# Performance work log

Hardware: AMD Instinct MI355X
Metric: run time of the kernel (lower is better)

Reference implementation:

```python
import jax, jax.numpy as jnp
import numpy as np

N_NODES = 50000
N_EDGES = 500000
D_IN = 128
HID = 128
OUT = 2
N_REL = 4
BN_EPS = 1e-5


def setup_inputs() -> dict:
    key = jax.random.key(0)
    ks = jax.random.split(key, 14)
    s_in = 1.0 / np.sqrt(D_IN)
    s_h = 1.0 / np.sqrt(HID)
    return {
        "x": jax.random.normal(ks[0], (N_NODES, D_IN), jnp.float32),
        "edge_index": jax.random.randint(ks[1], (N_REL, 2, N_EDGES), 0, N_NODES, jnp.int32),
        "W1": jax.random.normal(ks[2], (N_REL, D_IN, HID), jnp.float32) * s_in,
        "b1": jax.random.normal(ks[3], (N_REL, HID), jnp.float32) * s_in,
        "W2": jax.random.normal(ks[4], (N_REL, HID, HID), jnp.float32) * s_h,
        "b2": jax.random.normal(ks[5], (N_REL, HID), jnp.float32) * s_h,
        "bn_gamma": jnp.ones((HID,), jnp.float32),
        "bn_beta": jnp.zeros((HID,), jnp.float32),
        "lin1_W": jax.random.normal(ks[6], (HID, HID), jnp.float32) * s_h,
        "lin1_b": jax.random.normal(ks[7], (HID,), jnp.float32) * s_h,
        "lin2_W": jax.random.normal(ks[8], (HID, OUT), jnp.float32) * s_h,
        "lin2_b": jax.random.normal(ks[9], (OUT,), jnp.float32) * s_h,
    }


def _gcn(x, ei, W, b):
    # GCNConv: D^-1/2 (A + I) D^-1/2 (X W) + b
    n = x.shape[0]
    h = x @ W                                    # [N, H]
    loops = jnp.arange(n, dtype=ei.dtype)
    src = jnp.concatenate([ei[0], loops])        # add self loops
    dst = jnp.concatenate([ei[1], loops])
    deg = jax.ops.segment_sum(jnp.ones(dst.shape, h.dtype), dst, num_segments=n)
    dinv = jnp.where(deg > 0, jax.lax.rsqrt(deg), 0.0)
    norm = dinv[src] * dinv[dst]                 # [E+N]
    msg = h[src] * norm[:, None]                 # gather + scale
    return jax.ops.segment_sum(msg, dst, num_segments=n) + b


def _hetero(x, edge_index, W, b):
    # HeteroConv with aggr='sum' over the 4 relation types (same src/dst node type)
    out = _gcn(x, edge_index[0], W[0], b[0])
    for r in range(1, N_REL):
        out = out + _gcn(x, edge_index[r], W[r], b[r])
    return out


def reference(x, edge_index, W1, b1, W2, b2, bn_gamma, bn_beta, lin1_W, lin1_b, lin2_W, lin2_b):
    h = jax.nn.relu(_hetero(x, edge_index, W1, b1))
    h = jax.nn.relu(_hetero(h, edge_index, W2, b2))
    # BatchNorm1d (batch statistics, biased variance)
    mean = h.mean(axis=0)
    var = h.var(axis=0)
    h = (h - mean) * jax.lax.rsqrt(var + BN_EPS) * bn_gamma + bn_beta
    h = jax.nn.relu(h @ lin1_W + lin1_b)
    # dropout is identity in eval
    return h @ lin2_W + lin2_b
```

## Files before the change

kernel.cpp:

```cpp
#include <hip/hip_runtime.h>
#include <math.h>

#define NN 50000
#define NE 500000
#define NREL 4
#define D 128
#define RSZ 512
#define NRANGE 98
#define NBK (NREL * NRANGE)
#define BCAP 6144
#define NCH 128
#define CH 3907
#define FCAP 96
#define CAST_BLKS 6250
static constexpr float BN_EPS = 1e-5f;

typedef __attribute__((ext_vector_type(8))) short short8;
typedef __attribute__((ext_vector_type(4))) float f32x4;

__device__ __forceinline__ float bf2f(unsigned short u) {
    return __uint_as_float(((unsigned)u) << 16);
}
__device__ __forceinline__ unsigned short f2bf(float f) {
    unsigned x = __float_as_uint(f);
    return (unsigned short)((x + 0x7FFFu + ((x >> 16) & 1u)) >> 16);
}

__global__ __launch_bounds__(256) void k_pre(const float* __restrict__ x,
                                             const float* __restrict__ W1, const float* __restrict__ W2,
                                             const float* __restrict__ l1W, const float* __restrict__ b1,
                                             const float* __restrict__ b2,
                                             unsigned short* __restrict__ xb,
                                             unsigned short* __restrict__ Wt1,
                                             unsigned short* __restrict__ Wt2,
                                             unsigned short* __restrict__ Wt3,
                                             float* __restrict__ bs1, float* __restrict__ bs2,
                                             float* __restrict__ bnsum) {
    int blk = blockIdx.x, tid = threadIdx.x;
    if (blk < CAST_BLKS) {
        int i = blk * 256 + tid;
        float4 v = *(const float4*)(x + (size_t)i * 4);
        unsigned short u[4] = {f2bf(v.x), f2bf(v.y), f2bf(v.z), f2bf(v.w)};
        *(ushort4*)(xb + (size_t)i * 4) = *(ushort4*)u;
    } else if (blk < CAST_BLKS + 256) {
        int i = (blk - CAST_BLKS) * 256 + tid;
        int kk = i & 511, n = i >> 9;
        Wt1[n * 512 + kk] = f2bf(W1[kk * 128 + n]);
        Wt2[n * 512 + kk] = f2bf(W2[kk * 128 + n]);
    } else if (blk < CAST_BLKS + 320) {
        int i = (blk - CAST_BLKS - 256) * 256 + tid;
        int kk = i & 127, n = i >> 7;
        Wt3[n * 128 + kk] = f2bf(l1W[kk * 128 + n]);
    } else {
        if (tid < 128) {
            bs1[tid] = b1[tid] + b1[128 + tid] + b1[256 + tid] + b1[384 + tid];
            bs2[tid] = b2[tid] + b2[128 + tid] + b2[256 + tid] + b2[384 + tid];
        }
        bnsum[tid] = 0.f;
    }
}

__global__ __launch_bounds__(256) void k_bin(const int* __restrict__ ei,
                                             int* __restrict__ frag,
                                             int* __restrict__ cntg) {
    int c = blockIdx.x, r = blockIdx.y;
    const int* srcp = ei + r * 2 * NE;
    const int* dstp = srcp + NE;
    __shared__ int bins[NRANGE * FCAP];
    __shared__ int cnt[NRANGE];
    int tid = threadIdx.x;
    for (int i = tid; i < NRANGE; i += 256) cnt[i] = 0;
    __syncthreads();
    int e0 = c * CH, e1 = min(e0 + CH, NE);
    for (int e = e0 + tid; e < e1; e += 256) {
        int d = dstp[e];
        int s = srcp[e];
        int q = d >> 9;
        int pos = atomicAdd(&cnt[q], 1);
        if (pos < FCAP) bins[q * FCAP + pos] = s | ((d & 511) << 16);
    }
    __syncthreads();
    int w = tid >> 6, lane = tid & 63;
    for (int q = w; q < NRANGE; q += 4) {
        int k = min(cnt[q], FCAP);
        int gbase = ((r * NRANGE + q) * NCH + c) * FCAP;
        for (int i = lane; i < k; i += 64) frag[gbase + i] = bins[q * FCAP + i];
    }
    for (int q = tid; q < NRANGE; q += 256) cntg[(r * NRANGE + q) * NCH + c] = min(cnt[q], FCAP);
}

__global__ __launch_bounds__(512) void k_sortb(const int* __restrict__ frag,
                                               const int* __restrict__ cntg,
                                               unsigned short* __restrict__ csr,
                                               int* __restrict__ rstart,
                                               int* __restrict__ rend,
                                               float* __restrict__ dinv) {
    int q = blockIdx.x, r = blockIdx.y;
    int blk = r * NRANGE + q;
    int n0 = q * RSZ;
    int nrows = min(RSZ, NN - n0);
    __shared__ int cnts[NCH], cbase[NCH];
    __shared__ int stage[BCAP];
    __shared__ unsigned short csr_s[BCAP];
    __shared__ int hist[RSZ], off[RSZ], cnt2[RSZ];
    int tid = threadIdx.x;
    hist[tid] = 0;
    cnt2[tid] = 0;
    if (tid < NCH) cnts[tid] = cntg[blk * NCH + tid];
    __syncthreads();
    if (tid < NCH) cbase[tid] = cnts[tid];
    __syncthreads();
    for (int d = 1; d < NCH; d <<= 1) {
        int t = 0;
        if (tid < NCH && tid >= d) t = cbase[tid - d];
        __syncthreads();
        if (tid < NCH) cbase[tid] += t;
        __syncthreads();
    }
    if (tid < NCH) cbase[tid] -= cnts[tid];
    __syncthreads();
    int tot = cbase[NCH - 1] + cnts[NCH - 1];
    {
        int g = tid >> 2, l = tid & 3;
        int k = cnts[g], cb = cbase[g];
        int gbase = (blk * NCH + g) * FCAP;
        for (int i = l; i < k; i += 4)
            if (cb + i < BCAP) stage[cb + i] = frag[gbase + i];
    }
    __syncthreads();
    if (tot > BCAP) tot = BCAP;
    for (int i = tid; i < tot; i += 512) atomicAdd(&hist[(stage[i] >> 16) & 511], 1);
    __syncthreads();
    int h = hist[tid];
    if (tid < nrows) dinv[r * NN + n0 + tid] = rsqrtf((float)(h + 1));
    off[tid] = h;
    __syncthreads();
    for (int d = 1; d < RSZ; d <<= 1) {
        int t = (tid >= d) ? off[tid - d] : 0;
        __syncthreads();
        off[tid] += t;
        __syncthreads();
    }
    int excl = off[tid] - h;
    __syncthreads();
    off[tid] = excl;
    int base = blk * BCAP;
    if (tid < nrows) {
        rstart[r * NN + n0 + tid] = base + excl;
        rend[r * NN + n0 + tid] = base + excl + h;
    }
    __syncthreads();
    for (int i = tid; i < tot; i += 512) {
        int v = stage[i];
        int dl = (v >> 16) & 511;
        int p = atomicAdd(&cnt2[dl], 1);
        csr_s[off[dl] + p] = (unsigned short)(v & 0xFFFF);
    }
    __syncthreads();
    for (int i = tid; i < tot; i += 512) csr[base + i] = csr_s[i];
}

__global__ __launch_bounds__(256) void k_agg(const unsigned short* __restrict__ in,
                                             const unsigned short* __restrict__ csr,
                                             const int* __restrict__ rstart,
                                             const int* __restrict__ rend,
                                             const float* __restrict__ dinv,
                                             unsigned short* __restrict__ Acat) {
    int r = blockIdx.y;
    int wave = threadIdx.x >> 6, lane = threadIdx.x & 63;
    int n = blockIdx.x * 4 + wave;
    if (n >= NN) return;
    const float* dv = dinv + r * NN;
    int start = rstart[r * NN + n], end = rend[r * NN + n];
    int half = lane >> 5;
    int c = lane & 31;
    const ushort4* in4 = (const ushort4*)in;
    float a0 = 0.f, a1 = 0.f, a2 = 0.f, a3 = 0.f;
    int e = start + half;
    for (; e + 2 < end; e += 4) {
        int s0 = csr[e], s1 = csr[e + 2];
        float w0 = dv[s0], w1 = dv[s1];
        ushort4 u0 = in4[s0 * 32 + c];
        ushort4 u1 = in4[s1 * 32 + c];
        a0 = fmaf(bf2f(u0.x), w0, a0); a1 = fmaf(bf2f(u0.y), w0, a1);
        a2 = fmaf(bf2f(u0.z), w0, a2); a3 = fmaf(bf2f(u0.w), w0, a3);
        a0 = fmaf(bf2f(u1.x), w1, a0); a1 = fmaf(bf2f(u1.y), w1, a1);
        a2 = fmaf(bf2f(u1.z), w1, a2); a3 = fmaf(bf2f(u1.w), w1, a3);
    }
    if (e < end) {
        int s = csr[e];
        float w = dv[s];
        ushort4 u = in4[s * 32 + c];
        a0 = fmaf(bf2f(u.x), w, a0); a1 = fmaf(bf2f(u.y), w, a1);
        a2 = fmaf(bf2f(u.z), w, a2); a3 = fmaf(bf2f(u.w), w, a3);
    }
    a0 += __shfl_xor(a0, 32); a1 += __shfl_xor(a1, 32);
    a2 += __shfl_xor(a2, 32); a3 += __shfl_xor(a3, 32);
    float wn = dv[n];
    ushort4 us = in4[n * 32 + c];
    unsigned short ob[4];
    ob[0] = f2bf(wn * fmaf(bf2f(us.x), wn, a0));
    ob[1] = f2bf(wn * fmaf(bf2f(us.y), wn, a1));
    ob[2] = f2bf(wn * fmaf(bf2f(us.z), wn, a2));
    ob[3] = f2bf(wn * fmaf(bf2f(us.w), wn, a3));
    if (half == 0)
        *(ushort4*)(Acat + (size_t)n * 512 + r * 128 + 4 * c) = *(ushort4*)ob;
}

template <int K, bool STATS>
__global__ __launch_bounds__(256) void k_mm(const unsigned short* __restrict__ A,
                                            const unsigned short* __restrict__ Bt,
                                            const float* __restrict__ bias,
                                            unsigned short* __restrict__ C,
                                            float* __restrict__ bnsum) {
    int tid = threadIdx.x;
    int w = tid >> 6, lane = tid & 63;
    int ln = lane & 15, quad = lane >> 4;
    int mwave = blockIdx.x * 256 + w * 64;

    f32x4 acc[4][8];
#pragma unroll
    for (int a = 0; a < 4; a++)
#pragma unroll
        for (int b = 0; b < 8; b++) acc[a][b] = (f32x4){0.f, 0.f, 0.f, 0.f};

    size_t arow[4];
#pragma unroll
    for (int mf = 0; mf < 4; mf++) {
        int m = mwave + mf * 16 + ln;
        arow[mf] = (size_t)min(m, NN - 1) * K;
    }
    size_t brow[8];
#pragma unroll
    for (int nf = 0; nf < 8; nf++) brow[nf] = (size_t)(nf * 16 + ln) * K;

    for (int k0 = 0; k0 < K; k0 += 32) {
        int kof = k0 + quad * 8;
        short8 af[4], bf[8];
#pragma unroll
        for (int mf = 0; mf < 4; mf++) af[mf] = *(const short8*)(A + arow[mf] + kof);
#pragma unroll
        for (int nf = 0; nf < 8; nf++) bf[nf] = *(const short8*)(Bt + brow[nf] + kof);
#pragma unroll
        for (int mf = 0; mf < 4; mf++)
#pragma unroll
            for (int nf = 0; nf < 8; nf++)
                acc[mf][nf] = __builtin_amdgcn_mfma_f32_16x16x32_bf16(af[mf], bf[nf], acc[mf][nf], 0, 0, 0);
    }

    float bs[8];
#pragma unroll
    for (int nf = 0; nf < 8; nf++) bs[nf] = bias[nf * 16 + ln];
    float sn[8], qn[8];
#pragma unroll
    for (int nf = 0; nf < 8; nf++) { sn[nf] = 0.f; qn[nf] = 0.f; }

#pragma unroll
    for (int mf = 0; mf < 4; mf++)
#pragma unroll
        for (int nf = 0; nf < 8; nf++)
#pragma unroll
            for (int rg = 0; rg < 4; rg++) {
                int m = mwave + mf * 16 + quad * 4 + rg;
                if (m < NN) {
                    float v = fmaxf(acc[mf][nf][rg] + bs[nf], 0.f);
                    if (STATS) { sn[nf] += v; qn[nf] += v * v; }
                    C[(size_t)m * 128 + nf * 16 + ln] = f2bf(v);
                }
            }

    if (STATS) {
#pragma unroll
        for (int nf = 0; nf < 8; nf++) {
            float s = sn[nf], q = qn[nf];
            s += __shfl_xor(s, 16); s += __shfl_xor(s, 32);
            q += __shfl_xor(q, 16); q += __shfl_xor(q, 32);
            if (quad == 0) {
                unsafeAtomicAdd(&bnsum[nf * 16 + ln], s);
                unsafeAtomicAdd(&bnsum[128 + nf * 16 + ln], q);
            }
        }
    }
}

__global__ __launch_bounds__(256) void k_final(const unsigned short* __restrict__ R2,
                                               const float* __restrict__ bnsum,
                                               const float* __restrict__ gamma,
                                               const float* __restrict__ beta,
                                               const unsigned short* __restrict__ Wt3,
                                               const float* __restrict__ l1b,
                                               const float* __restrict__ l2W,
                                               const float* __restrict__ l2b,
                                               float* __restrict__ out) {
    __shared__ float bnp_s[256];
    int tid = threadIdx.x;
    if (tid < 128) {
        float mean = bnsum[tid] / (float)NN;
        float var = bnsum[128 + tid] / (float)NN - mean * mean;
        float sc = gamma[tid] * rsqrtf(var + BN_EPS);
        bnp_s[tid] = sc;
        bnp_s[128 + tid] = beta[tid] - mean * sc;
    }
    __syncthreads();
    int w = tid >> 6, lane = tid & 63;
    int ln = lane & 15, quad = lane >> 4;
    int mwave = blockIdx.x * 256 + w * 64;

    f32x4 acc[4][8];
#pragma unroll
    for (int a = 0; a < 4; a++)
#pragma unroll
        for (int b = 0; b < 8; b++) acc[a][b] = (f32x4){0.f, 0.f, 0.f, 0.f};

    size_t arow[4];
#pragma unroll
    for (int mf = 0; mf < 4; mf++) {
        int m = mwave + mf * 16 + ln;
        arow[mf] = (size_t)min(m, NN - 1) * 128;
    }
    size_t brow[8];
#pragma unroll
    for (int nf = 0; nf < 8; nf++) brow[nf] = (size_t)(nf * 16 + ln) * 128;

    for (int k0 = 0; k0 < 128; k0 += 32) {
        int kof = k0 + quad * 8;
        float scv[8], shv[8];
#pragma unroll
        for (int j = 0; j < 8; j++) {
            scv[j] = bnp_s[kof + j];
            shv[j] = bnp_s[128 + kof + j];
        }
        short8 af[4], bf[8];
#pragma unroll
        for (int mf = 0; mf < 4; mf++) {
            short8 rv = *(const short8*)(R2 + arow[mf] + kof);
            unsigned short ab[8];
#pragma unroll
            for (int j = 0; j < 8; j++)
                ab[j] = f2bf(bf2f((unsigned short)rv[j]) * scv[j] + shv[j]);
            af[mf] = *(short8*)ab;
        }
#pragma unroll
        for (int nf = 0; nf < 8; nf++) bf[nf] = *(const short8*)(Wt3 + brow[nf] + kof);
#pragma unroll
        for (int mf = 0; mf < 4; mf++)
#pragma unroll
            for (int nf = 0; nf < 8; nf++)
                acc[mf][nf] = __builtin_amdgcn_mfma_f32_16x16x32_bf16(af[mf], bf[nf], acc[mf][nf], 0, 0, 0);
    }

    float b1v[8], w0[8], w1[8];
#pragma unroll
    for (int nf = 0; nf < 8; nf++) {
        int n = nf * 16 + ln;
        b1v[nf] = l1b[n];
        w0[nf] = l2W[n * 2];
        w1[nf] = l2W[n * 2 + 1];
    }
    float ob0 = l2b[0], ob1 = l2b[1];
#pragma unroll
    for (int mf = 0; mf < 4; mf++)
#pragma unroll
        for (int rg = 0; rg < 4; rg++) {
            float p0 = 0.f, p1 = 0.f;
#pragma unroll
            for (int nf = 0; nf < 8; nf++) {
                float y = fmaxf(acc[mf][nf][rg] + b1v[nf], 0.f);
                p0 += y * w0[nf];
                p1 += y * w1[nf];
            }
            p0 += __shfl_xor(p0, 1); p0 += __shfl_xor(p0, 2);
            p0 += __shfl_xor(p0, 4); p0 += __shfl_xor(p0, 8);
            p1 += __shfl_xor(p1, 1); p1 += __shfl_xor(p1, 2);
            p1 += __shfl_xor(p1, 4); p1 += __shfl_xor(p1, 8);
            int m = mwave + mf * 16 + quad * 4 + rg;
            if (ln == 0 && m < NN) {
                out[(size_t)m * 2 + 0] = p0 + ob0;
                out[(size_t)m * 2 + 1] = p1 + ob1;
            }
        }
}

extern "C" void kernel_launch(void* const* d_in, const int* in_sizes, int n_in,
                              void* d_out, int out_size, void* d_ws, size_t ws_size,
                              hipStream_t stream) {
    const float* x = (const float*)d_in[0];
    const int* ei = (const int*)d_in[1];
    const float* W1 = (const float*)d_in[2];
    const float* b1 = (const float*)d_in[3];
    const float* W2 = (const float*)d_in[4];
    const float* b2 = (const float*)d_in[5];
    const float* gamma = (const float*)d_in[6];
    const float* beta = (const float*)d_in[7];
    const float* l1W = (const float*)d_in[8];
    const float* l1b = (const float*)d_in[9];
    const float* l2W = (const float*)d_in[10];
    const float* l2b = (const float*)d_in[11];
    float* out = (float*)d_out;

    char* ws = (char*)d_ws;
    size_t off = 0;
    auto alloc = [&](size_t bytes) {
        void* p = ws + off;
        off += (bytes + 255) & ~(size_t)255;
        return p;
    };
    float* dinv = (float*)alloc((size_t)NREL * NN * sizeof(float));
    int* rstart = (int*)alloc((size_t)NREL * NN * sizeof(int));
    int* rend = (int*)alloc((size_t)NREL * NN * sizeof(int));
    unsigned short* csr = (unsigned short*)alloc((size_t)NBK * BCAP * 2);
    unsigned short* xb = (unsigned short*)alloc((size_t)NN * D * 2);
    unsigned short* Acat = (unsigned short*)alloc((size_t)NN * 512 * 2);
    unsigned short* h1b = (unsigned short*)alloc((size_t)NN * D * 2);
    unsigned short* R2b = (unsigned short*)alloc((size_t)NN * D * 2);
    unsigned short* Wt1 = (unsigned short*)alloc(128 * 512 * 2);
    unsigned short* Wt2 = (unsigned short*)alloc(128 * 512 * 2);
    unsigned short* Wt3 = (unsigned short*)alloc(128 * 128 * 2);
    float* bs1 = (float*)alloc(128 * sizeof(float));
    float* bs2 = (float*)alloc(128 * sizeof(float));
    float* bnsum = (float*)alloc(256 * sizeof(float));

    int* frag = (int*)Acat;
    int* cntg = frag + (size_t)NREL * NRANGE * NCH * FCAP;

    k_pre<<<CAST_BLKS + 321, 256, 0, stream>>>(x, W1, W2, l1W, b1, b2, xb, Wt1, Wt2, Wt3,
                                               bs1, bs2, bnsum);
    dim3 bgrid(NCH, NREL);
    k_bin<<<bgrid, 256, 0, stream>>>(ei, frag, cntg);
    dim3 sgrid(NRANGE, NREL);
    k_sortb<<<sgrid, 512, 0, stream>>>(frag, cntg, csr, rstart, rend, dinv);

    dim3 agrid((NN + 3) / 4, NREL);
    k_agg<<<agrid, 256, 0, stream>>>(xb, csr, rstart, rend, dinv, Acat);
    k_mm<512, false><<<(NN + 255) / 256, 256, 0, stream>>>(Acat, Wt1, bs1, h1b, nullptr);
    k_agg<<<agrid, 256, 0, stream>>>(h1b, csr, rstart, rend, dinv, Acat);
    k_mm<512, true><<<(NN + 255) / 256, 256, 0, stream>>>(Acat, Wt2, bs2, R2b, bnsum);
    k_final<<<(NN + 255) / 256, 256, 0, stream>>>(R2b, bnsum, gamma, beta, Wt3, l1b, l2W, l2b, out);
}
```

Baseline: 428.8 us.

## Precompute per-edge weights and restructure aggregation with wave-cooperative neighbor loads

Adds a kernel that precomputes each CSR entry's source normalization weight (dinv[src]) into a float array stored in the otherwise-unused R2b buffer. The aggregation kernel now loads up to 64 neighbor indices and weights coalesced per wave and broadcasts them with shuffles. Four edges are processed concurrently, each 16-lane group fetching a full 128-feature row with 16-byte loads. This removes the dependent random dinv gather and widens the feature loads, at the cost of an extra kernel pass over the CSR, more shuffles, and a 4-way cross-lane reduction.

```diff
diff --git a/kernel.cpp b/kernel.cpp
--- a/kernel.cpp
+++ b/kernel.cpp
@@ -160,8 +160,18 @@
     for (int i = tid; i < tot; i += 512) csr[base + i] = csr_s[i];
 }
 
+__global__ __launch_bounds__(256) void k_wei(const unsigned short* __restrict__ csr,
+                                             const float* __restrict__ dinv,
+                                             float* __restrict__ wcsr) {
+    int gi = blockIdx.x * 256 + threadIdx.x;
+    int r = gi / (NRANGE * BCAP);
+    int s = csr[gi];
+    wcsr[gi] = dinv[r * NN + min(s, NN - 1)];
+}
+
 __global__ __launch_bounds__(256) void k_agg(const unsigned short* __restrict__ in,
                                              const unsigned short* __restrict__ csr,
+                                             const float* __restrict__ wcsr,
                                              const int* __restrict__ rstart,
                                              const int* __restrict__ rend,
                                              const float* __restrict__ dinv,
@@ -170,41 +180,57 @@
     int wave = threadIdx.x >> 6, lane = threadIdx.x & 63;
     int n = blockIdx.x * 4 + wave;
     if (n >= NN) return;
-    const float* dv = dinv + r * NN;
-    int start = rstart[r * NN + n], end = rend[r * NN + n];
-    int half = lane >> 5;
-    int c = lane & 31;
-    const ushort4* in4 = (const ushort4*)in;
-    float a0 = 0.f, a1 = 0.f, a2 = 0.f, a3 = 0.f;
-    int e = start + half;
-    for (; e + 2 < end; e += 4) {
-        int s0 = csr[e], s1 = csr[e + 2];
-        float w0 = dv[s0], w1 = dv[s1];
-        ushort4 u0 = in4[s0 * 32 + c];
-        ushort4 u1 = in4[s1 * 32 + c];
-        a0 = fmaf(bf2f(u0.x), w0, a0); a1 = fmaf(bf2f(u0.y), w0, a1);
-        a2 = fmaf(bf2f(u0.z), w0, a2); a3 = fmaf(bf2f(u0.w), w0, a3);
-        a0 = fmaf(bf2f(u1.x), w1, a0); a1 = fmaf(bf2f(u1.y), w1, a1);
-        a2 = fmaf(bf2f(u1.z), w1, a2); a3 = fmaf(bf2f(u1.w), w1, a3);
-    }
-    if (e < end) {
-        int s = csr[e];
-        float w = dv[s];
-        ushort4 u = in4[s * 32 + c];
-        a0 = fmaf(bf2f(u.x), w, a0); a1 = fmaf(bf2f(u.y), w, a1);
-        a2 = fmaf(bf2f(u.z), w, a2); a3 = fmaf(bf2f(u.w), w, a3);
-    }
-    a0 += __shfl_xor(a0, 32); a1 += __shfl_xor(a1, 32);
-    a2 += __shfl_xor(a2, 32); a3 += __shfl_xor(a3, 32);
-    float wn = dv[n];
-    ushort4 us = in4[n * 32 + c];
-    unsigned short ob[4];
-    ob[0] = f2bf(wn * fmaf(bf2f(us.x), wn, a0));
-    ob[1] = f2bf(wn * fmaf(bf2f(us.y), wn, a1));
-    ob[2] = f2bf(wn * fmaf(bf2f(us.z), wn, a2));
-    ob[3] = f2bf(wn * fmaf(bf2f(us.w), wn, a3));
-    if (half == 0)
-        *(ushort4*)(Acat + (size_t)n * 512 + r * 128 + 4 * c) = *(ushort4*)ob;
+    int nb = r * NN + n;
+    int start = rstart[nb], end = rend[nb];
+    int deg = end - start;
+    int q = lane >> 4, t = lane & 15;
+    const short8* in8 = (const short8*)in;
+    float a[8];
+#pragma unroll
+    for (int j = 0; j < 8; j++) a[j] = 0.f;
+    for (int w0 = 0; w0 < deg; w0 += 64) {
+        int li = w0 + lane;
+        int sv = 0;
+        float wv = 0.f;
+        if (li < deg) {
+            sv = csr[start + li];
+            wv = wcsr[start + li];
+        }
+        int cnt = min(deg - w0, 64);
+        for (int b = 0; b < cnt; b += 16) {
+            int e = b + q * 4;
+            int s0 = __shfl(sv, e + 0), s1 = __shfl(sv, e + 1);
+            int s2 = __shfl(sv, e + 2), s3 = __shfl(sv, e + 3);
+            float f0 = __shfl(wv, e + 0), f1 = __shfl(wv, e + 1);
+            float f2 = __shfl(wv, e + 2), f3 = __shfl(wv, e + 3);
+            short8 u0 = in8[s0 * 16 + t];
+            short8 u1 = in8[s1 * 16 + t];
+            short8 u2 = in8[s2 * 16 + t];
+            short8 u3 = in8[s3 * 16 + t];
+#pragma unroll
+            for (int j = 0; j < 8; j++) a[j] = fmaf(bf2f((unsigned short)u0[j]), f0, a[j]);
+#pragma unroll
+            for (int j = 0; j < 8; j++) a[j] = fmaf(bf2f((unsigned short)u1[j]), f1, a[j]);
+#pragma unroll
+            for (int j = 0; j < 8; j++) a[j] = fmaf(bf2f((unsigned short)u2[j]), f2, a[j]);
+#pragma unroll
+            for (int j = 0; j < 8; j++) a[j] = fmaf(bf2f((unsigned short)u3[j]), f3, a[j]);
+        }
+    }
+#pragma unroll
+    for (int j = 0; j < 8; j++) {
+        a[j] += __shfl_xor(a[j], 16);
+        a[j] += __shfl_xor(a[j], 32);
+    }
+    if (q == 0) {
+        float wn = dinv[nb];
+        short8 us = in8[n * 16 + t];
+        unsigned short ob[8];
+#pragma unroll
+        for (int j = 0; j < 8; j++)
+            ob[j] = f2bf(wn * fmaf(bf2f((unsigned short)us[j]), wn, a[j]));
+        *(short8*)(Acat + (size_t)n * 512 + r * 128 + t * 8) = *(short8*)ob;
+    }
 }
 
 template <int K, bool STATS>
@@ -422,6 +448,7 @@
 
     int* frag = (int*)Acat;
     int* cntg = frag + (size_t)NREL * NRANGE * NCH * FCAP;
+    float* wcsr = (float*)R2b;
 
     k_pre<<<CAST_BLKS + 321, 256, 0, stream>>>(x, W1, W2, l1W, b1, b2, xb, Wt1, Wt2, Wt3,
                                                bs1, bs2, bnsum);
@@ -429,11 +456,12 @@
     k_bin<<<bgrid, 256, 0, stream>>>(ei, frag, cntg);
     dim3 sgrid(NRANGE, NREL);
     k_sortb<<<sgrid, 512, 0, stream>>>(frag, cntg, csr, rstart, rend, dinv);
+    k_wei<<<(NBK * BCAP) / 256, 256, 0, stream>>>(csr, dinv, wcsr);
 
     dim3 agrid((NN + 3) / 4, NREL);
-    k_agg<<<agrid, 256, 0, stream>>>(xb, csr, rstart, rend, dinv, Acat);
+    k_agg<<<agrid, 256, 0, stream>>>(xb, csr, wcsr, rstart, rend, dinv, Acat);
     k_mm<512, false><<<(NN + 255) / 256, 256, 0, stream>>>(Acat, Wt1, bs1, h1b, nullptr);
-    k_agg<<<agrid, 256, 0, stream>>>(h1b, csr, rstart, rend, dinv, Acat);
+    k_agg<<<agrid, 256, 0, stream>>>(h1b, csr, wcsr, rstart, rend, dinv, Acat);
     k_mm<512, true><<<(NN + 255) / 256, 256, 0, stream>>>(Acat, Wt2, bs2, R2b, bnsum);
     k_final<<<(NN + 255) / 256, 256, 0, stream>>>(R2b, bnsum, gamma, beta, Wt3, l1b, l2W, l2b, out);
 }
```

After: 396.0 us. -7.6%, faster.
